# Kernel tuning notes

Hardware: AMD Instinct MI355X
Metric: run time of the kernel (lower is better)

The kernel has to match this reference:

```python
import jax, jax.numpy as jnp
import numpy as np

B, C, H, W, K, HD = 4, 64, 128, 128, 9, 64


def conv1x1(x, w, b):
    # x: [N,Ci,H,W], w: [Co,Ci], b: [Co]
    return jnp.einsum('oc,bchw->bohw', w, x) + b[None, :, None, None]


def dsconv(x, dw, pw, pb):
    # depthwise 1x1 (per-channel scale) then pointwise 1x1
    return conv1x1(x * dw[None, :, None, None], pw, pb)


def bilinear_sample(x, gx, gy):
    # x: [B,C,H,W]; gx,gy: [B,K,H,W] normalized grid coords in torch convention.
    # Matches F.grid_sample(mode='bilinear', padding_mode='zeros', align_corners=False).
    b, c, h, w = x.shape
    k = gx.shape[1]
    ix = ((gx + 1.0) * w - 1.0) * 0.5
    iy = ((gy + 1.0) * h - 1.0) * 0.5
    x0 = jnp.floor(ix)
    y0 = jnp.floor(iy)
    wx = (ix - x0)[:, None]  # [B,1,K,H,W]
    wy = (iy - y0)[:, None]
    x0i = x0.astype(jnp.int32)
    y0i = y0.astype(jnp.int32)
    xf = x.reshape(b, c, h * w)

    def gather(yi, xi):
        valid = ((yi >= 0) & (yi < h) & (xi >= 0) & (xi < w))
        idx = (jnp.clip(yi, 0, h - 1) * w + jnp.clip(xi, 0, w - 1)).reshape(b, 1, -1)
        v = jnp.take_along_axis(xf, idx, axis=2).reshape(b, c, k, h, w)
        return v * valid.astype(x.dtype).reshape(b, 1, k, h, w)

    v00 = gather(y0i, x0i)
    v01 = gather(y0i, x0i + 1)
    v10 = gather(y0i + 1, x0i)
    v11 = gather(y0i + 1, x0i + 1)
    return (v00 * (1 - wy) * (1 - wx) + v01 * (1 - wy) * wx
            + v10 * wy * (1 - wx) + v11 * wy * wx)  # [B,C,K,H,W]


def setup_inputs() -> dict:
    key = jax.random.key(0)
    ks = jax.random.split(key, 16)
    d = {
        'x': jax.random.normal(ks[0], (B, C, H, W), jnp.float32),
        'alpha': jnp.array([0.5], jnp.float32),
        'off_w': jax.random.normal(ks[1], (2 * K, C), jnp.float32) * 0.05,
        'off_b': jax.random.normal(ks[2], (2 * K,), jnp.float32) * 0.05,
        'q_dw': jax.random.normal(ks[3], (C,), jnp.float32) * (1.0 / np.sqrt(C)),
        'q_pw': jax.random.normal(ks[4], (HD, C), jnp.float32) * (1.0 / np.sqrt(C)),
        'q_pb': jnp.zeros((HD,), jnp.float32),
        'k_dw': jax.random.normal(ks[5], (C,), jnp.float32) * (1.0 / np.sqrt(C)),
        'k_pw': jax.random.normal(ks[6], (HD, C), jnp.float32) * (1.0 / np.sqrt(C)),
        'k_pb': jnp.zeros((HD,), jnp.float32),
        'v_dw': jax.random.normal(ks[7], (C,), jnp.float32) * (1.0 / np.sqrt(C)),
        'v_pw': jax.random.normal(ks[8], (HD, C), jnp.float32) * (1.0 / np.sqrt(C)),
        'v_pb': jnp.zeros((HD,), jnp.float32),
        'o_dw': jax.random.normal(ks[9], (HD,), jnp.float32) * (1.0 / np.sqrt(HD)),
        'o_pw': jax.random.normal(ks[10], (C, HD), jnp.float32) * (1.0 / np.sqrt(HD)),
        'o_pb': jnp.zeros((C,), jnp.float32),
    }
    return d


def reference(x, alpha, off_w, off_b, q_dw, q_pw, q_pb, k_dw, k_pw, k_pb,
              v_dw, v_pw, v_pb, o_dw, o_pw, o_pb):
    b, c, h, w = x.shape
    offsets = conv1x1(x, off_w, off_b).reshape(b, 2, K, h, w)
    dx, dy = offsets[:, 0], offsets[:, 1]  # [B,K,H,W]
    yy = jnp.arange(h, dtype=x.dtype)[None, None, :, None]
    xx = jnp.arange(w, dtype=x.dtype)[None, None, None, :]
    gy = 2.0 * (yy + dy) / (h - 1) - 1.0
    gx = 2.0 * (xx + dx) / (w - 1) - 1.0
    sampled = bilinear_sample(x, gx, gy)  # [B,C,K,H,W]
    samp_flat = sampled.transpose(0, 2, 1, 3, 4).reshape(b * K, c, h, w)
    Kf = dsconv(samp_flat, k_dw, k_pw, k_pb).reshape(b, K, HD, h, w)
    Vf = dsconv(samp_flat, v_dw, v_pw, v_pb).reshape(b, K, HD, h, w)
    Q = dsconv(x, q_dw, q_pw, q_pb)  # [B,HD,H,W]
    scores = jnp.einsum('bchw,bkchw->bkhw', Q, Kf)
    attn = jax.nn.softmax(scores, axis=1)
    wV = jnp.einsum('bkhw,bkchw->bchw', attn, Vf)
    out = alpha[0] * wV + Q
    return dsconv(out, o_dw, o_pw, o_pb)
```

## Files before the change

### kernel.cpp

```cpp
#include <hip/hip_runtime.h>

#define HW (128*128)
#define CHW (64*HW)

typedef _Float16 h2 __attribute__((ext_vector_type(2)));
typedef _Float16 h4 __attribute__((ext_vector_type(4)));
typedef _Float16 h8 __attribute__((ext_vector_type(8)));
typedef float f32x4 __attribute__((ext_vector_type(4)));

union H8P { h8 v; h2 p[4]; };
union H4P { h4 v; h2 p[2]; int2 i; };

#if !__has_builtin(__builtin_amdgcn_fdot2)
__device__ __forceinline__ float __builtin_amdgcn_fdot2(h2 a, h2 b, float c, bool) {
  return c + (float)a[0]*(float)b[0] + (float)a[1]*(float)b[1];
}
#endif

__global__ __launch_bounds__(256) void prep_kernel(
    const float* __restrict__ x, _Float16* __restrict__ xt,
    const float* __restrict__ alpha,
    const float* __restrict__ q_dw, const float* __restrict__ q_pw, const float* __restrict__ q_pb,
    const float* __restrict__ k_dw, const float* __restrict__ k_pw,
    const float* __restrict__ offw, const float* __restrict__ offb,
    const float* __restrict__ v_dw, const float* __restrict__ v_pw, const float* __restrict__ v_pb,
    const float* __restrict__ o_dw, const float* __restrict__ o_pw, const float* __restrict__ o_pb,
    _Float16* __restrict__ Apack2, _Float16* __restrict__ Apack6,
    float* __restrict__ bias96, float* __restrict__ boutd)
{
  int tid = threadIdx.x;
  if (blockIdx.x < 1024) {
    __shared__ __align__(16) float t[64][68];
    int i0 = blockIdx.x;
    int blk = (i0 & 7)*128 + (i0 >> 3);
    int b = blk >> 8; int y = (blk >> 1) & 127; int x0 = (blk & 1) << 6;
    const float* xb = x + b*CHW + y*128 + x0;
    {
      int c = tid >> 2, q = tid & 3;
      const float4* srcv = (const float4*)(xb + c*HW + q*16);
      float4* dst = (float4*)&t[c][q*16];
      #pragma unroll
      for (int i = 0; i < 4; ++i) dst[i] = srcv[i];
    }
    __syncthreads();
    {
      int p = tid >> 2, hc = tid & 3;
      h8 o0, o1;
      #pragma unroll
      for (int j = 0; j < 8; ++j) o0[j] = (_Float16)t[hc*16 + j][p];
      #pragma unroll
      for (int j = 0; j < 8; ++j) o1[j] = (_Float16)t[hc*16 + 8 + j][p];
      h8* dstg = (h8*)(xt + (size_t)(b*HW + y*128 + x0 + p)*64 + hc*16);
      dstg[0] = o0; dstg[1] = o1;
    }
    return;
  }
  int bb = blockIdx.x - 1024;
  float a = alpha[0];
  if (bb < 24) {
    int e = bb*256 + tid;
    int j = e & 7, l = (e >> 3) & 63, kt = (e >> 9) & 1, mt = e >> 10;
    int row = mt*16 + (l & 15);
    int c   = kt*32 + (l >> 4)*8 + j;
    float v = 0.f;
    if (row < 64) {
      float s = 0.f;
      for (int o = 0; o < 64; ++o) s += k_pw[o*64+row]*q_pw[o*64+c];
      v = k_dw[row]*q_dw[c]*s;
    } else if (row < 82) {
      v = offw[(row-64)*64 + c];
    }
    Apack2[e] = (_Float16)v;
  } else if (bb < 56) {
    int e = (bb-24)*256 + tid;
    int j = e & 7, l = (e >> 3) & 63, kt = (e >> 9) & 3, mt = e >> 11;
    int o  = mt*16 + (l & 15);
    int cc = kt*32 + (l >> 4)*8 + j;
    float v;
    if (cc < 64) {
      float s = 0.f;
      for (int h = 0; h < 64; ++h) s += o_pw[o*64+h]*o_dw[h]*v_pw[h*64+cc];
      v = a*v_dw[cc]*s;
    } else {
      int c2 = cc - 64;
      float s = 0.f;
      for (int h = 0; h < 64; ++h) s += o_pw[o*64+h]*o_dw[h]*q_pw[h*64+c2];
      v = q_dw[c2]*s;
    }
    Apack6[e] = (_Float16)v;
  } else {
    if (tid < 96) {
      float v = 0.f;
      if (tid < 64) {
        float s = 0.f;
        for (int o = 0; o < 64; ++o) s += k_pw[o*64+tid]*q_pb[o];
        v = k_dw[tid]*s;
      } else if (tid < 82) {
        v = offb[tid-64];
      }
      bias96[tid] = v;
    } else if (tid >= 128 && tid < 192) {
      int o = tid - 128;
      float s2 = 0.f;
      for (int h = 0; h < 64; ++h) s2 += o_pw[o*64+h]*o_dw[h]*(a*v_pb[h]+q_pb[h]);
      boutd[o] = o_pb[o] + s2;
    }
  }
}

__global__ __launch_bounds__(256, 5) void dam_kernel(
  const _Float16* __restrict__ xt,
  const _Float16* __restrict__ Apack2, const _Float16* __restrict__ Apack6,
  const float* __restrict__ bias96, const float* __restrict__ boutd,
  float* __restrict__ out)
{
  __shared__ __align__(16) char lds[16128];
  _Float16 (*xs)[72]  = (_Float16 (*)[72])lds;
  _Float16 (*qkL)[72] = (_Float16 (*)[72])(lds + 4608);
  _Float16 (*qs)[72]  = (_Float16 (*)[72])(lds + 4608);
  float (*offsF)[32]  = (float (*)[32])(lds + 9216);
  int4* prm           = (int4*)(lds + 11520);

  int i0 = blockIdx.x;
  int blk = (i0 & 7)*256 + (i0 >> 3);
  int b = blk >> 9; int y = (blk >> 2) & 127; int x0 = (blk & 3) << 5;
  int tid = threadIdx.x;
  int g = tid >> 6;
  int wg = __builtin_amdgcn_readfirstlane(g);
  int lane = tid & 63;

  {
    const h8* src = (const h8*)(xt + (size_t)(b*HW + y*128 + x0)*64);
    h8 v = src[tid];
    *(h8*)&xs[tid >> 3][(tid & 7)*8] = v;
  }
  __syncthreads();

  {
    const h8* A2 = (const h8*)Apack2;
    #pragma unroll
    for (int i = 0; i < 3; ++i) {
      int t = wg*3 + i; int m = t >> 1, n = t & 1;
      int row0 = m*16 + (lane >> 4)*4;
      int pcol = n*16 + (lane & 15);
      f32x4 acc;
      #pragma unroll
      for (int r = 0; r < 4; ++r) acc[r] = bias96[row0 + r];
      h8 b0 = *(const h8*)&xs[pcol][(lane >> 4)*8];
      h8 b1 = *(const h8*)&xs[pcol][32 + (lane >> 4)*8];
      acc = __builtin_amdgcn_mfma_f32_16x16x32_f16(A2[(m*2+0)*64 + lane], b0, acc, 0, 0, 0);
      acc = __builtin_amdgcn_mfma_f32_16x16x32_f16(A2[(m*2+1)*64 + lane], b1, acc, 0, 0, 0);
      if (m < 4) {
        h4 v;
        #pragma unroll
        for (int r = 0; r < 4; ++r) v[r] = (_Float16)acc[r];
        *(h4*)&qkL[pcol][m*16 + (lane >> 4)*4] = v;
      } else {
        #pragma unroll
        for (int r = 0; r < 4; ++r) {
          int row = row0 + r;
          if (row < 82) offsF[row - 64][pcol] = acc[r];
        }
      }
    }
  }
  __syncthreads();

  #pragma unroll
  for (int pass = 0; pass < 2; ++pass) {
    int e = tid + pass*256;
    if (e < 288) {
      int k = e >> 5, pp = e & 31;
      float dx = offsF[k][pp];
      float dy = offsF[9+k][pp];
      float fx = (float)(x0 + pp);
      float fy = (float)y;
      float gx = 2.0f*(fx + dx)/127.0f - 1.0f;
      float gy = 2.0f*(fy + dy)/127.0f - 1.0f;
      float ix = ((gx + 1.0f)*128.0f - 1.0f)*0.5f;
      float iy = ((gy + 1.0f)*128.0f - 1.0f)*0.5f;
      float x0f = floorf(ix), y0f = floorf(iy);
      float wx = ix - x0f, wy = iy - y0f;
      int xi = (int)x0f, yi = (int)y0f;
      bool vx0 = (xi >= 0) && (xi < 128);
      bool vx1 = (xi >= -1) && (xi < 127);
      bool vy0 = (yi >= 0) && (yi < 128);
      bool vy1 = (yi >= -1) && (yi < 127);
      H4P w;
      w.v[0] = (_Float16)((1.f-wy)*(1.f-wx)*((vy0&&vx0)?1.f:0.f));
      w.v[1] = (_Float16)((1.f-wy)*wx      *((vy0&&vx1)?1.f:0.f));
      w.v[2] = (_Float16)(wy*(1.f-wx)      *((vy1&&vx0)?1.f:0.f));
      w.v[3] = (_Float16)(wy*wx            *((vy1&&vx1)?1.f:0.f));
      int xc0 = min(max(xi,0),127), xc1 = min(max(xi+1,0),127);
      int yc0 = min(max(yi,0),127), yc1 = min(max(yi+1,0),127);
      int4 pr;
      pr.x = (yc0*128 + xc0)*64;
      pr.y = (xc1 - xc0)*64 | (((yc1 - yc0)*8192) << 16);
      pr.z = w.i.x;
      pr.w = w.i.y;
      prm[e] = pr;
    }
  }
  int pxl = wg*8 + (lane >> 3);
  int ch8 = (lane & 7)*8;
  H8P qkh; qkh.v = *(const h8*)&qkL[pxl][ch8];
  __syncthreads();

  const _Float16* xtb = xt + (size_t)b*HW*64 + ch8;

  h2 smp[9][4];
  float sarr[9];
  #pragma unroll
  for (int kb = 0; kb < 3; ++kb) {
    int4 pr[3];
    #pragma unroll
    for (int u = 0; u < 3; ++u) pr[u] = prm[(kb*3+u)*32 + pxl];
    H8P A[3], Bc[3], Cc[3], D[3];
    #pragma unroll
    for (int u = 0; u < 3; ++u) {
      int dxs = pr[u].y & 0xFFFF;
      int dys = pr[u].y >> 16;
      const _Float16* base = xtb + pr[u].x;
      A[u].v  = *(const h8*)(base);
      Bc[u].v = *(const h8*)(base + dxs);
      Cc[u].v = *(const h8*)(base + dys);
      D[u].v  = *(const h8*)(base + dys + dxs);
    }
    #pragma unroll
    for (int u = 0; u < 3; ++u) {
      int k = kb*3 + u;
      H4P w; w.i.x = pr[u].z; w.i.y = pr[u].w;
      h2 w0h; w0h[0] = w.v[0]; w0h[1] = w.v[0];
      h2 w1h; w1h[0] = w.v[1]; w1h[1] = w.v[1];
      h2 w2h; w2h[0] = w.v[2]; w2h[1] = w.v[2];
      h2 w3h; w3h[0] = w.v[3]; w3h[1] = w.v[3];
      float s = 0.f;
      #pragma unroll
      for (int j = 0; j < 4; ++j) {
        h2 v = A[u].p[j]*w0h + Bc[u].p[j]*w1h + Cc[u].p[j]*w2h + D[u].p[j]*w3h;
        smp[k][j] = v;
        s = __builtin_amdgcn_fdot2(v, qkh.p[j], s, false);
      }
      s += __shfl_xor(s, 1, 64);
      s += __shfl_xor(s, 2, 64);
      s += __shfl_xor(s, 4, 64);
      sarr[k] = s;
    }
  }

  float m = sarr[0];
  #pragma unroll
  for (int k = 1; k < 9; ++k) m = fmaxf(m, sarr[k]);
  float ssum = 0.f;
  #pragma unroll
  for (int k = 0; k < 9; ++k) { float e2 = __expf(sarr[k]-m); ssum += e2; sarr[k] = e2; }
  float inv = 1.f/ssum;

  h2 S2[4];
  #pragma unroll
  for (int j = 0; j < 4; ++j) { S2[j][0] = (_Float16)0.f; S2[j][1] = (_Float16)0.f; }
  #pragma unroll
  for (int k = 0; k < 9; ++k) {
    _Float16 akh = (_Float16)(sarr[k]*inv);
    h2 ak; ak[0] = akh; ak[1] = akh;
    #pragma unroll
    for (int j = 0; j < 4; ++j) S2[j] = S2[j] + ak*smp[k][j];
  }
  __syncthreads();
  {
    H8P sv;
    sv.p[0] = S2[0]; sv.p[1] = S2[1]; sv.p[2] = S2[2]; sv.p[3] = S2[3];
    *(h8*)&qs[pxl][ch8] = sv.v;
  }
  __syncthreads();

  {
    const h8* A6 = (const h8*)Apack6;
    float* ob = out + b*CHW + y*128 + x0;
    #pragma unroll
    for (int i = 0; i < 2; ++i) {
      int t = wg*2 + i; int m2 = t >> 1, n = t & 1;
      int row0 = m2*16 + (lane >> 4)*4;
      int pcol = n*16 + (lane & 15);
      f32x4 acc;
      #pragma unroll
      for (int r = 0; r < 4; ++r) acc[r] = boutd[row0 + r];
      h8 b0 = *(const h8*)&qs[pcol][(lane >> 4)*8];
      h8 b1 = *(const h8*)&qs[pcol][32 + (lane >> 4)*8];
      h8 b2 = *(const h8*)&xs[pcol][(lane >> 4)*8];
      h8 b3 = *(const h8*)&xs[pcol][32 + (lane >> 4)*8];
      acc = __builtin_amdgcn_mfma_f32_16x16x32_f16(A6[(m2*4+0)*64 + lane], b0, acc, 0, 0, 0);
      acc = __builtin_amdgcn_mfma_f32_16x16x32_f16(A6[(m2*4+1)*64 + lane], b1, acc, 0, 0, 0);
      acc = __builtin_amdgcn_mfma_f32_16x16x32_f16(A6[(m2*4+2)*64 + lane], b2, acc, 0, 0, 0);
      acc = __builtin_amdgcn_mfma_f32_16x16x32_f16(A6[(m2*4+3)*64 + lane], b3, acc, 0, 0, 0);
      #pragma unroll
      for (int r = 0; r < 4; ++r) ob[(row0 + r)*HW + pcol] = acc[r];
    }
  }
}

extern "C" void kernel_launch(void* const* d_in, const int* in_sizes, int n_in,
                              void* d_out, int out_size, void* d_ws, size_t ws_size,
                              hipStream_t stream)
{
  const float* x    = (const float*)d_in[0];
  const float* alpha= (const float*)d_in[1];
  const float* offw = (const float*)d_in[2];
  const float* offb = (const float*)d_in[3];
  const float* q_dw = (const float*)d_in[4];
  const float* q_pw = (const float*)d_in[5];
  const float* q_pb = (const float*)d_in[6];
  const float* k_dw = (const float*)d_in[7];
  const float* k_pw = (const float*)d_in[8];
  const float* v_dw = (const float*)d_in[10];
  const float* v_pw = (const float*)d_in[11];
  const float* v_pb = (const float*)d_in[12];
  const float* o_dw = (const float*)d_in[13];
  const float* o_pw = (const float*)d_in[14];
  const float* o_pb = (const float*)d_in[15];
  float* out = (float*)d_out;

  char* ws        = (char*)d_ws;
  _Float16* xt    = (_Float16*)ws;
  _Float16* Apack2= (_Float16*)(ws + (size_t)4*HW*64*2);
  _Float16* Apack6= Apack2 + 6144;
  float* bias96   = (float*)(Apack6 + 8192);
  float* boutd    = bias96 + 96;

  prep_kernel<<<1081, 256, 0, stream>>>(x, xt, alpha, q_dw, q_pw, q_pb, k_dw, k_pw,
                                        offw, offb, v_dw, v_pw, v_pb,
                                        o_dw, o_pw, o_pb,
                                        Apack2, Apack6, bias96, boutd);
  dam_kernel<<<2048, 256, 0, stream>>>(xt, Apack2, Apack6, bias96, boutd, out);
}
```

Before: 28.89 us.

## Double block size and split nine sampling points across thread pairs

The dam kernel now runs 512 threads per block instead of 256. Each pixel/channel-group is handled by two threads that split the nine deformable sample points 5/4, then exchange scores and partial weighted sums via lane shuffles. The MFMA stages are redistributed over 8 waves. The goal is more parallelism and memory-level concurrency for the gathers with fewer registers per thread, at the cost of extra shuffles, a larger block and a lower occupancy bound.

After: 37.89 us. 1.31x slower.

```diff
diff --git a/kernel.cpp b/kernel.cpp
--- a/kernel.cpp
+++ b/kernel.cpp
@@ -10,6 +10,7 @@
 
 union H8P { h8 v; h2 p[4]; };
 union H4P { h4 v; h2 p[2]; int2 i; };
+union HF  { h2 h; int i; };
 
 #if !__has_builtin(__builtin_amdgcn_fdot2)
 __device__ __forceinline__ float __builtin_amdgcn_fdot2(h2 a, h2 b, float c, bool) {
@@ -108,7 +109,7 @@
   }
 }
 
-__global__ __launch_bounds__(256, 5) void dam_kernel(
+__global__ __launch_bounds__(512, 4) void dam_kernel(
   const _Float16* __restrict__ xt,
   const _Float16* __restrict__ Apack2, const _Float16* __restrict__ Apack6,
   const float* __restrict__ bias96, const float* __restrict__ boutd,
@@ -129,7 +130,7 @@
   int wg = __builtin_amdgcn_readfirstlane(g);
   int lane = tid & 63;
 
-  {
+  if (tid < 256) {
     const h8* src = (const h8*)(xt + (size_t)(b*HW + y*128 + x0)*64);
     h8 v = src[tid];
     *(h8*)&xs[tid >> 3][(tid & 7)*8] = v;
@@ -139,85 +140,89 @@
   {
     const h8* A2 = (const h8*)Apack2;
     #pragma unroll
-    for (int i = 0; i < 3; ++i) {
-      int t = wg*3 + i; int m = t >> 1, n = t & 1;
-      int row0 = m*16 + (lane >> 4)*4;
-      int pcol = n*16 + (lane & 15);
-      f32x4 acc;
-      #pragma unroll
-      for (int r = 0; r < 4; ++r) acc[r] = bias96[row0 + r];
-      h8 b0 = *(const h8*)&xs[pcol][(lane >> 4)*8];
-      h8 b1 = *(const h8*)&xs[pcol][32 + (lane >> 4)*8];
-      acc = __builtin_amdgcn_mfma_f32_16x16x32_f16(A2[(m*2+0)*64 + lane], b0, acc, 0, 0, 0);
-      acc = __builtin_amdgcn_mfma_f32_16x16x32_f16(A2[(m*2+1)*64 + lane], b1, acc, 0, 0, 0);
-      if (m < 4) {
-        h4 v;
+    for (int i = 0; i < 2; ++i) {
+      int t = wg + i*8;
+      if (t < 12) {
+        int m = t >> 1, n = t & 1;
+        int row0 = m*16 + (lane >> 4)*4;
+        int pcol = n*16 + (lane & 15);
+        f32x4 acc;
         #pragma unroll
-        for (int r = 0; r < 4; ++r) v[r] = (_Float16)acc[r];
-        *(h4*)&qkL[pcol][m*16 + (lane >> 4)*4] = v;
-      } else {
-        #pragma unroll
-        for (int r = 0; r < 4; ++r) {
-          int row = row0 + r;
-          if (row < 82) offsF[row - 64][pcol] = acc[r];
+        for (int r = 0; r < 4; ++r) acc[r] = bias96[row0 + r];
+        h8 b0 = *(const h8*)&xs[pcol][(lane >> 4)*8];
+        h8 b1 = *(const h8*)&xs[pcol][32 + (lane >> 4)*8];
+        acc = __builtin_amdgcn_mfma_f32_16x16x32_f16(A2[(m*2+0)*64 + lane], b0, acc, 0, 0, 0);
+        acc = __builtin_amdgcn_mfma_f32_16x16x32_f16(A2[(m*2+1)*64 + lane], b1, acc, 0, 0, 0);
+        if (m < 4) {
+          h4 v;
+          #pragma unroll
+          for (int r = 0; r < 4; ++r) v[r] = (_Float16)acc[r];
+          *(h4*)&qkL[pcol][m*16 + (lane >> 4)*4] = v;
+        } else {
+          #pragma unroll
+          for (int r = 0; r < 4; ++r) {
+            int row = row0 + r;
+            if (row < 82) offsF[row - 64][pcol] = acc[r];
+          }
         }
       }
     }
   }
   __syncthreads();
 
-  #pragma unroll
-  for (int pass = 0; pass < 2; ++pass) {
-    int e = tid + pass*256;
-    if (e < 288) {
-      int k = e >> 5, pp = e & 31;
-      float dx = offsF[k][pp];
-      float dy = offsF[9+k][pp];
-      float fx = (float)(x0 + pp);
-      float fy = (float)y;
-      float gx = 2.0f*(fx + dx)/127.0f - 1.0f;
-      float gy = 2.0f*(fy + dy)/127.0f - 1.0f;
-      float ix = ((gx + 1.0f)*128.0f - 1.0f)*0.5f;
-      float iy = ((gy + 1.0f)*128.0f - 1.0f)*0.5f;
-      float x0f = floorf(ix), y0f = floorf(iy);
-      float wx = ix - x0f, wy = iy - y0f;
-      int xi = (int)x0f, yi = (int)y0f;
-      bool vx0 = (xi >= 0) && (xi < 128);
-      bool vx1 = (xi >= -1) && (xi < 127);
-      bool vy0 = (yi >= 0) && (yi < 128);
-      bool vy1 = (yi >= -1) && (yi < 127);
-      H4P w;
-      w.v[0] = (_Float16)((1.f-wy)*(1.f-wx)*((vy0&&vx0)?1.f:0.f));
-      w.v[1] = (_Float16)((1.f-wy)*wx      *((vy0&&vx1)?1.f:0.f));
-      w.v[2] = (_Float16)(wy*(1.f-wx)      *((vy1&&vx0)?1.f:0.f));
-      w.v[3] = (_Float16)(wy*wx            *((vy1&&vx1)?1.f:0.f));
-      int xc0 = min(max(xi,0),127), xc1 = min(max(xi+1,0),127);
-      int yc0 = min(max(yi,0),127), yc1 = min(max(yi+1,0),127);
-      int4 pr;
-      pr.x = (yc0*128 + xc0)*64;
-      pr.y = (xc1 - xc0)*64 | (((yc1 - yc0)*8192) << 16);
-      pr.z = w.i.x;
-      pr.w = w.i.y;
-      prm[e] = pr;
-    }
-  }
-  int pxl = wg*8 + (lane >> 3);
-  int ch8 = (lane & 7)*8;
-  H8P qkh; qkh.v = *(const h8*)&qkL[pxl][ch8];
+  if (tid < 288) {
+    int e = tid;
+    int k = e >> 5, pp = e & 31;
+    float dx = offsF[k][pp];
+    float dy = offsF[9+k][pp];
+    float fx = (float)(x0 + pp);
+    float fy = (float)y;
+    float gx = 2.0f*(fx + dx)/127.0f - 1.0f;
+    float gy = 2.0f*(fy + dy)/127.0f - 1.0f;
+    float ix = ((gx + 1.0f)*128.0f - 1.0f)*0.5f;
+    float iy = ((gy + 1.0f)*128.0f - 1.0f)*0.5f;
+    float x0f = floorf(ix), y0f = floorf(iy);
+    float wx = ix - x0f, wy = iy - y0f;
+    int xi = (int)x0f, yi = (int)y0f;
+    bool vx0 = (xi >= 0) && (xi < 128);
+    bool vx1 = (xi >= -1) && (xi < 127);
+    bool vy0 = (yi >= 0) && (yi < 128);
+    bool vy1 = (yi >= -1) && (yi < 127);
+    H4P w;
+    w.v[0] = (_Float16)((1.f-wy)*(1.f-wx)*((vy0&&vx0)?1.f:0.f));
+    w.v[1] = (_Float16)((1.f-wy)*wx      *((vy0&&vx1)?1.f:0.f));
+    w.v[2] = (_Float16)(wy*(1.f-wx)      *((vy1&&vx0)?1.f:0.f));
+    w.v[3] = (_Float16)(wy*wx            *((vy1&&vx1)?1.f:0.f));
+    int xc0 = min(max(xi,0),127), xc1 = min(max(xi+1,0),127);
+    int yc0 = min(max(yi,0),127), yc1 = min(max(yi+1,0),127);
+    int4 pr;
+    pr.x = (yc0*128 + xc0)*64;
+    pr.y = (xc1 - xc0)*64 | (((yc1 - yc0)*8192) << 16);
+    pr.z = w.i.x;
+    pr.w = w.i.y;
+    prm[e] = pr;
+  }
+  int px  = tid >> 4;
+  int sub = tid & 15;
+  int kg  = sub >> 3;
+  int ch8 = (sub & 7)*8;
+  int nk  = kg ? 4 : 5;
+  int k0  = kg ? 5 : 0;
+  H8P qkh; qkh.v = *(const h8*)&qkL[px][ch8];
   __syncthreads();
 
   const _Float16* xtb = xt + (size_t)b*HW*64 + ch8;
 
-  h2 smp[9][4];
-  float sarr[9];
-  #pragma unroll
-  for (int kb = 0; kb < 3; ++kb) {
-    int4 pr[3];
-    #pragma unroll
-    for (int u = 0; u < 3; ++u) pr[u] = prm[(kb*3+u)*32 + pxl];
-    H8P A[3], Bc[3], Cc[3], D[3];
-    #pragma unroll
-    for (int u = 0; u < 3; ++u) {
+  h2 smp[5][4];
+  float sloc[5];
+  int4 pr[5];
+  #pragma unroll
+  for (int u = 0; u < 5; ++u)
+    if (u < nk) pr[u] = prm[(k0+u)*32 + px];
+  H8P A[5], Bc[5], Cc[5], D[5];
+  #pragma unroll
+  for (int u = 0; u < 5; ++u) {
+    if (u < nk) {
       int dxs = pr[u].y & 0xFFFF;
       int dys = pr[u].y >> 16;
       const _Float16* base = xtb + pr[u].x;
@@ -226,9 +231,10 @@
       Cc[u].v = *(const h8*)(base + dys);
       D[u].v  = *(const h8*)(base + dys + dxs);
     }
-    #pragma unroll
-    for (int u = 0; u < 3; ++u) {
-      int k = kb*3 + u;
+  }
+  #pragma unroll
+  for (int u = 0; u < 5; ++u) {
+    if (u < nk) {
       H4P w; w.i.x = pr[u].z; w.i.y = pr[u].w;
       h2 w0h; w0h[0] = w.v[0]; w0h[1] = w.v[0];
       h2 w1h; w1h[0] = w.v[1]; w1h[1] = w.v[1];
@@ -238,14 +244,32 @@
       #pragma unroll
       for (int j = 0; j < 4; ++j) {
         h2 v = A[u].p[j]*w0h + Bc[u].p[j]*w1h + Cc[u].p[j]*w2h + D[u].p[j]*w3h;
-        smp[k][j] = v;
+        smp[u][j] = v;
         s = __builtin_amdgcn_fdot2(v, qkh.p[j], s, false);
       }
       s += __shfl_xor(s, 1, 64);
       s += __shfl_xor(s, 2, 64);
       s += __shfl_xor(s, 4, 64);
-      sarr[k] = s;
-    }
+      sloc[u] = s;
+    } else {
+      sloc[u] = -1e30f;
+    }
+  }
+
+  float rec[5];
+  #pragma unroll
+  for (int j = 0; j < 5; ++j) rec[j] = __shfl_xor(sloc[j], 8, 64);
+  float sarr[9];
+  if (kg == 0) {
+    #pragma unroll
+    for (int k = 0; k < 5; ++k) sarr[k] = sloc[k];
+    #pragma unroll
+    for (int j = 0; j < 4; ++j) sarr[5+j] = rec[j];
+  } else {
+    #pragma unroll
+    for (int j = 0; j < 5; ++j) sarr[j] = rec[j];
+    #pragma unroll
+    for (int j = 0; j < 4; ++j) sarr[5+j] = sloc[j];
   }
 
   float m = sarr[0];
@@ -260,42 +284,47 @@
   #pragma unroll
   for (int j = 0; j < 4; ++j) { S2[j][0] = (_Float16)0.f; S2[j][1] = (_Float16)0.f; }
   #pragma unroll
-  for (int k = 0; k < 9; ++k) {
-    _Float16 akh = (_Float16)(sarr[k]*inv);
-    h2 ak; ak[0] = akh; ak[1] = akh;
-    #pragma unroll
-    for (int j = 0; j < 4; ++j) S2[j] = S2[j] + ak*smp[k][j];
-  }
-  __syncthreads();
-  {
+  for (int u = 0; u < 5; ++u) {
+    if (u < nk) {
+      _Float16 akh = (_Float16)(sarr[k0+u]*inv);
+      h2 ak; ak[0] = akh; ak[1] = akh;
+      #pragma unroll
+      for (int j = 0; j < 4; ++j) S2[j] = S2[j] + ak*smp[u][j];
+    }
+  }
+  #pragma unroll
+  for (int j = 0; j < 4; ++j) {
+    HF u2; u2.h = S2[j];
+    HF r2; r2.i = __shfl_xor(u2.i, 8, 64);
+    S2[j] = S2[j] + r2.h;
+  }
+  __syncthreads();
+  if (kg == 0) {
     H8P sv;
     sv.p[0] = S2[0]; sv.p[1] = S2[1]; sv.p[2] = S2[2]; sv.p[3] = S2[3];
-    *(h8*)&qs[pxl][ch8] = sv.v;
+    *(h8*)&qs[px][ch8] = sv.v;
   }
   __syncthreads();
 
   {
     const h8* A6 = (const h8*)Apack6;
     float* ob = out + b*CHW + y*128 + x0;
-    #pragma unroll
-    for (int i = 0; i < 2; ++i) {
-      int t = wg*2 + i; int m2 = t >> 1, n = t & 1;
-      int row0 = m2*16 + (lane >> 4)*4;
-      int pcol = n*16 + (lane & 15);
-      f32x4 acc;
-      #pragma unroll
-      for (int r = 0; r < 4; ++r) acc[r] = boutd[row0 + r];
-      h8 b0 = *(const h8*)&qs[pcol][(lane >> 4)*8];
-      h8 b1 = *(const h8*)&qs[pcol][32 + (lane >> 4)*8];
-      h8 b2 = *(const h8*)&xs[pcol][(lane >> 4)*8];
-      h8 b3 = *(const h8*)&xs[pcol][32 + (lane >> 4)*8];
-      acc = __builtin_amdgcn_mfma_f32_16x16x32_f16(A6[(m2*4+0)*64 + lane], b0, acc, 0, 0, 0);
-      acc = __builtin_amdgcn_mfma_f32_16x16x32_f16(A6[(m2*4+1)*64 + lane], b1, acc, 0, 0, 0);
-      acc = __builtin_amdgcn_mfma_f32_16x16x32_f16(A6[(m2*4+2)*64 + lane], b2, acc, 0, 0, 0);
-      acc = __builtin_amdgcn_mfma_f32_16x16x32_f16(A6[(m2*4+3)*64 + lane], b3, acc, 0, 0, 0);
-      #pragma unroll
-      for (int r = 0; r < 4; ++r) ob[(row0 + r)*HW + pcol] = acc[r];
-    }
+    int t = wg; int m2 = t >> 1, n = t & 1;
+    int row0 = m2*16 + (lane >> 4)*4;
+    int pcol = n*16 + (lane & 15);
+    f32x4 acc;
+    #pragma unroll
+    for (int r = 0; r < 4; ++r) acc[r] = boutd[row0 + r];
+    h8 b0 = *(const h8*)&qs[pcol][(lane >> 4)*8];
+    h8 b1 = *(const h8*)&qs[pcol][32 + (lane >> 4)*8];
+    h8 b2 = *(const h8*)&xs[pcol][(lane >> 4)*8];
+    h8 b3 = *(const h8*)&xs[pcol][32 + (lane >> 4)*8];
+    acc = __builtin_amdgcn_mfma_f32_16x16x32_f16(A6[(m2*4+0)*64 + lane], b0, acc, 0, 0, 0);
+    acc = __builtin_amdgcn_mfma_f32_16x16x32_f16(A6[(m2*4+1)*64 + lane], b1, acc, 0, 0, 0);
+    acc = __builtin_amdgcn_mfma_f32_16x16x32_f16(A6[(m2*4+2)*64 + lane], b2, acc, 0, 0, 0);
+    acc = __builtin_amdgcn_mfma_f32_16x16x32_f16(A6[(m2*4+3)*64 + lane], b3, acc, 0, 0, 0);
+    #pragma unroll
+    for (int r = 0; r < 4; ++r) ob[(row0 + r)*HW + pcol] = acc[r];
   }
 }
 
@@ -331,5 +360,5 @@
                                         offw, offb, v_dw, v_pw, v_pb,
                                         o_dw, o_pw, o_pb,
                                         Apack2, Apack6, bias96, boutd);
-  dam_kernel<<<2048, 256, 0, stream>>>(xt, Apack2, Apack6, bias96, boutd, out);
+  dam_kernel<<<2048, 512, 0, stream>>>(xt, Apack2, Apack6, bias96, boutd, out);
 }
```
